# Optimization experiments

Measured on AMD Instinct MI355X. Metric: run time of the kernel, lower is better.

Reference implementation:

```python
import jax, jax.numpy as jnp
import numpy as np

DIM = 1024
HEADS = 8
DIM_HEAD = 64
INNER = HEADS * DIM_HEAD  # 512


def setup_inputs() -> dict:
    key = jax.random.key(0)
    k1, k2, k3, k4 = jax.random.split(key, 4)
    x = jax.random.normal(k1, (4, 4096, DIM), dtype=jnp.float32)
    W_qkv = jax.random.normal(k2, (DIM, 3 * INNER), dtype=jnp.float32) * (DIM ** -0.5)
    W_out = jax.random.normal(k3, (INNER, DIM), dtype=jnp.float32) * (INNER ** -0.5)
    b_out = jax.random.normal(k4, (DIM,), dtype=jnp.float32) * 0.01
    return {"x": x, "W_qkv": W_qkv, "W_out": W_out, "b_out": b_out}


def reference(x, W_qkv, W_out, b_out):
    b, n, _ = x.shape
    qkv = x @ W_qkv                                   # [b, n, 3*inner]
    q, k, v = jnp.split(qkv, 3, axis=-1)              # each [b, n, inner]

    def to_heads(t):
        return t.reshape(b, n, HEADS, DIM_HEAD).transpose(0, 2, 1, 3)  # [b, h, n, d]

    q = jax.nn.elu(to_heads(q)) + 1.0
    k = jax.nn.elu(to_heads(k)) + 1.0
    v = to_heads(v)
    # kv summary matrix: [b, h, d, e]
    context = jnp.einsum('bhnd,bhne->bhde', k, v)
    out = jnp.einsum('bhde,bhnd->bhne', context, q)   # [b, h, n, e]
    out = out.transpose(0, 2, 1, 3).reshape(b, n, INNER)
    return out @ W_out + b_out
```

## Files before the change

kernel.cpp:

```cpp
#include <hip/hip_runtime.h>
#include <hip/hip_bf16.h>
#include <cstdint>

typedef __attribute__((ext_vector_type(4))) float f32x4;
typedef __attribute__((ext_vector_type(8))) short bf16x8;

__device__ __forceinline__ ushort f2bf(float f) {
  unsigned u = __builtin_bit_cast(unsigned, f);
  u += 0x7fffu + ((u >> 16) & 1u);
  return (ushort)(u >> 16);
}

__device__ __forceinline__ void gload_lds16(const ushort* g, ushort* l) {
  __builtin_amdgcn_global_load_lds(
      (const __attribute__((address_space(1))) unsigned int*)g,
      (__attribute__((address_space(3))) unsigned int*)l, 16, 0, 0);
}

__device__ __forceinline__ void hard_barrier() {
  __builtin_amdgcn_sched_barrier(0);
  __builtin_amdgcn_s_barrier();
  __builtin_amdgcn_sched_barrier(0);
}

template <int N>
__device__ __forceinline__ void wait_vm() {
  if constexpr (N == 0) asm volatile("s_waitcnt vmcnt(0)" ::: "memory");
  else if constexpr (N == 2) asm volatile("s_waitcnt vmcnt(2)" ::: "memory");
  else if constexpr (N == 4) asm volatile("s_waitcnt vmcnt(4)" ::: "memory");
  else if constexpr (N == 6) asm volatile("s_waitcnt vmcnt(6)" ::: "memory");
  else static_assert(N < 0, "unsupported vmcnt");
}

__device__ __forceinline__ float elu1(float v) {
  return (v > 0.f) ? (v + 1.f) : __expf(v);
}

__global__ __launch_bounds__(256) void prep_kernel(const float4* __restrict__ x,
                                                   ushort4* __restrict__ xb,
                                                   const float* __restrict__ W,
                                                   ushort* __restrict__ Wt) {
  if (blockIdx.x < 2048) {
    const int n4 = 16384 * 1024 / 4;
    const int stride = 2048 * 256;
    for (int i = blockIdx.x * 256 + threadIdx.x; i < n4; i += stride) {
      float4 f = x[i];
      ushort4 o;
      o.x = f2bf(f.x); o.y = f2bf(f.y); o.z = f2bf(f.z); o.w = f2bf(f.w);
      xb[i] = o;
    }
  } else {
    __shared__ float tile[32][33];
    const int tb = blockIdx.x - 2048;
    const int n0 = (tb % 48) * 32;
    const int k0 = (tb / 48) * 32;
    const int tx = threadIdx.x & 31;
    const int ty = threadIdx.x >> 5;
    #pragma unroll
    for (int p = 0; p < 4; ++p) {
      int k = k0 + ty + p * 8;
      tile[ty + p * 8][tx] = W[(size_t)k * 1536 + n0 + tx];
    }
    __syncthreads();
    #pragma unroll
    for (int p = 0; p < 4; ++p) {
      int n = n0 + ty + p * 8;
      Wt[(size_t)n * 1024 + k0 + tx] = f2bf(tile[tx][ty + p * 8]);
    }
  }
}

template <int LDA, int LDB, int NT>
__device__ __forceinline__ void gemm_core(const ushort* __restrict__ A,
                                          const ushort* __restrict__ Bt,
                                          int row0, int col0, f32x4 acc[4][4],
                                          ushort* lds) {
  const int tid = threadIdx.x;
  const int l = tid & 63;
  const int wid = tid >> 6;
  const int fr = l & 15;
  const int fq = l >> 4;
  const int wr = wid >> 2;
  const int wc = wid & 3;

  const int scol = ((l & 7) * 8) ^ (((l >> 3) & 7) * 8);
  const ushort* aS = A + (size_t)(row0 + (tid >> 3)) * LDA + scol;
  const ushort* bS = Bt + (size_t)(col0 + (tid >> 3)) * LDB + scol;

  int aRow[4], bRow[4], kx[2];
  #pragma unroll
  for (int m = 0; m < 4; ++m) aRow[m] = (wr * 64 + m * 16 + fr) * 64;
  #pragma unroll
  for (int n = 0; n < 4; ++n) bRow[n] = (wc * 64 + n * 16 + fr) * 64;
  #pragma unroll
  for (int ks = 0; ks < 2; ++ks) kx[ks] = (ks * 32 + fq * 8) ^ ((fr & 7) * 8);

  auto stage = [&](int t) {
    ushort* dst = lds + (t % 3) * 24576 + tid * 8;
    const int ko = t * 64;
    #pragma unroll
    for (int p = 0; p < 2; ++p)
      gload_lds16(aS + (size_t)(p * 64) * LDA + ko, dst + p * 4096);
    #pragma unroll
    for (int p = 0; p < 4; ++p)
      gload_lds16(bS + (size_t)(p * 64) * LDB + ko, dst + 8192 + p * 4096);
  };

  stage(0);
  stage(1);
  wait_vm<6>();
  hard_barrier();

  #pragma unroll
  for (int t = 0; t < NT; ++t) {
    if (t + 2 < NT) stage(t + 2);
    const ushort* aB = lds + (t % 3) * 24576;
    const ushort* bB = aB + 8192;
    #pragma unroll
    for (int ks = 0; ks < 2; ++ks) {
      bf16x8 av[4], bv[4];
      #pragma unroll
      for (int m = 0; m < 4; ++m) av[m] = *(const bf16x8*)&aB[aRow[m] + kx[ks]];
      #pragma unroll
      for (int n = 0; n < 4; ++n) bv[n] = *(const bf16x8*)&bB[bRow[n] + kx[ks]];
      __builtin_amdgcn_s_setprio(1);
      #pragma unroll
      for (int m = 0; m < 4; ++m)
        #pragma unroll
        for (int n = 0; n < 4; ++n)
          acc[m][n] = __builtin_amdgcn_mfma_f32_16x16x32_bf16(av[m], bv[n], acc[m][n], 0, 0, 0);
      __builtin_amdgcn_s_setprio(0);
    }
    if (t + 2 < NT) {
      wait_vm<6>();
      hard_barrier();
    } else if (t + 1 < NT) {
      wait_vm<0>();
      hard_barrier();
    }
  }
}

__global__ __launch_bounds__(512, 2) void gemm_qkv_kernel(const ushort* __restrict__ xb,
                                                          const ushort* __restrict__ wt,
                                                          ushort* __restrict__ q,
                                                          ushort* __restrict__ kT,
                                                          ushort* __restrict__ vT) {
  __shared__ ushort lds[73728];
  f32x4 acc[4][4] = {};
  const int row0 = blockIdx.x * 128;
  const int col0 = blockIdx.y * 256;
  gemm_core<1024, 1024, 16>(xb, wt, row0, col0, acc, lds);
  const int l = threadIdx.x & 63;
  const int wid = threadIdx.x >> 6;
  const int wr = wid >> 2, wc = wid & 3;
  const int fr = l & 15, fq = l >> 4;
  #pragma unroll
  for (int m = 0; m < 4; ++m) {
    #pragma unroll
    for (int n = 0; n < 4; ++n) {
      const int c = col0 + wc * 64 + n * 16 + fr;
      const int r0 = row0 + wr * 64 + m * 16 + fq * 4;
      if (c < 512) {
        #pragma unroll
        for (int j = 0; j < 4; ++j)
          q[(size_t)(r0 + j) * 512 + c] = f2bf(elu1(acc[m][n][j]));
      } else if (c < 1024) {
        const int d = c - 512;
        const int bh = (r0 >> 12) * 8 + (d >> 6);
        const int nn = r0 & 4095;
        ushort4 o;
        o.x = f2bf(elu1(acc[m][n][0]));
        o.y = f2bf(elu1(acc[m][n][1]));
        o.z = f2bf(elu1(acc[m][n][2]));
        o.w = f2bf(elu1(acc[m][n][3]));
        *(ushort4*)&kT[((size_t)bh * 64 + (d & 63)) * 4096 + nn] = o;
      } else {
        const int d = c - 1024;
        const int bh = (r0 >> 12) * 8 + (d >> 6);
        const int nn = r0 & 4095;
        ushort4 o;
        o.x = f2bf(acc[m][n][0]);
        o.y = f2bf(acc[m][n][1]);
        o.z = f2bf(acc[m][n][2]);
        o.w = f2bf(acc[m][n][3]);
        *(ushort4*)&vT[((size_t)bh * 64 + (d & 63)) * 4096 + nn] = o;
      }
    }
  }
}

__global__ __launch_bounds__(256) void ctx_mfma_kernel(const ushort* __restrict__ kT,
                                                       const ushort* __restrict__ vT,
                                                       float* __restrict__ part) {
  __shared__ ushort lds[16384];
  const int bh = blockIdx.x;
  const int sp = blockIdx.y;
  const int tid = threadIdx.x;
  const int l = tid & 63, wid = tid >> 6;
  const int fr = l & 15, fq = l >> 4;
  const int wr = wid >> 1, wc = wid & 1;

  const size_t base = (size_t)bh * 64 * 4096 + sp * 512;
  const int srow = tid >> 2;
  const int lam = (tid & 3) ^ ((tid >> 3) & 3);
  const ushort* aG = kT + base + (size_t)srow * 4096 + lam * 8;
  const ushort* bG = vT + base + (size_t)srow * 4096 + lam * 8;

  auto stage = [&](int t) {
    ushort* d = lds + (t & 3) * 4096 + tid * 8;
    gload_lds16(aG + t * 32, d);
    gload_lds16(bG + t * 32, d + 2048);
  };

  const int sig = fq ^ ((fr >> 1) & 3);
  f32x4 acc[2][2] = {};

  auto compute = [&](int t) {
    const ushort* sb = lds + (t & 3) * 4096;
    bf16x8 av[2], bv[2];
    #pragma unroll
    for (int mm = 0; mm < 2; ++mm)
      av[mm] = *(const bf16x8*)&sb[(wr * 32 + mm * 16 + fr) * 32 + sig * 8];
    #pragma unroll
    for (int nn = 0; nn < 2; ++nn)
      bv[nn] = *(const bf16x8*)&sb[2048 + (wc * 32 + nn * 16 + fr) * 32 + sig * 8];
    #pragma unroll
    for (int mm = 0; mm < 2; ++mm)
      #pragma unroll
      for (int nn = 0; nn < 2; ++nn)
        acc[mm][nn] = __builtin_amdgcn_mfma_f32_16x16x32_bf16(av[mm], bv[nn], acc[mm][nn], 0, 0, 0);
  };

  constexpr int NT = 16;
  stage(0); stage(1); stage(2);
  for (int t = 0; t < NT; ++t) {
    if (t <= NT - 3) wait_vm<4>();
    else if (t == NT - 2) wait_vm<2>();
    else wait_vm<0>();
    hard_barrier();
    compute(t);
    hard_barrier();
    if (t + 3 < NT) stage(t + 3);
  }

  float* dst = part + ((size_t)sp * 32 + bh) * 4096;
  #pragma unroll
  for (int mm = 0; mm < 2; ++mm)
    #pragma unroll
    for (int nn = 0; nn < 2; ++nn)
      #pragma unroll
      for (int j = 0; j < 4; ++j)
        dst[(wr * 32 + mm * 16 + fq * 4 + j) * 64 + wc * 32 + nn * 16 + fr] = acc[mm][nn][j];
}

__global__ __launch_bounds__(256) void weff_kernel(const float* __restrict__ part,
                                                   const float* __restrict__ Wout,
                                                   ushort* __restrict__ weff) {
  const int bh = blockIdx.x;
  const int h = bh & 7;
  const int m0 = blockIdx.y * 128;
  const int t = threadIdx.x;
  __shared__ float cs[64 * 64];
  __shared__ float ws[64][128];
  #pragma unroll
  for (int p = 0; p < 4; ++p) {
    const int idx = p * 1024 + t * 4;
    f32x4 s = {};
    #pragma unroll
    for (int sp = 0; sp < 8; ++sp)
      s += *(const f32x4*)&part[(size_t)sp * 131072 + (size_t)bh * 4096 + idx];
    *(f32x4*)&cs[idx] = s;
  }
  #pragma unroll
  for (int p = 0; p < 8; ++p) {
    const int e = (t >> 5) + p * 8;
    const int c = (t & 31) * 4;
    *(float4*)&ws[e][c] = *(const float4*)&Wout[(size_t)(h * 64 + e) * 1024 + m0 + c];
  }
  __syncthreads();
  const int m = t & 127;
  const int dh = (t >> 7) * 32;
  float acc[32] = {};
  for (int e = 0; e < 64; ++e) {
    const float w = ws[e][m];
    #pragma unroll
    for (int i = 0; i < 32; ++i)
      acc[i] += cs[(dh + i) * 64 + e] * w;
  }
  ushort* dst = weff + ((size_t)(bh >> 3) * 1024 + m0 + m) * 512 + h * 64 + dh;
  #pragma unroll
  for (int i = 0; i < 32; ++i) dst[i] = f2bf(acc[i]);
}

__global__ __launch_bounds__(512, 2) void gemm_out_kernel(const ushort* __restrict__ q,
                                                          const ushort* __restrict__ weff,
                                                          const float* __restrict__ bout,
                                                          float* __restrict__ out) {
  __shared__ ushort lds[73728];
  f32x4 acc[4][4] = {};
  const int row0 = blockIdx.x * 128;
  const int col0 = blockIdx.y * 256;
  const int b = row0 >> 12;
  gemm_core<512, 512, 8>(q, weff + (size_t)b * 1024 * 512, row0, col0, acc, lds);
  const int l = threadIdx.x & 63;
  const int wid = threadIdx.x >> 6;
  const int wr = wid >> 2, wc = wid & 3;
  const int fr = l & 15, fq = l >> 4;
  #pragma unroll
  for (int m = 0; m < 4; ++m) {
    #pragma unroll
    for (int n = 0; n < 4; ++n) {
      const int c = col0 + wc * 64 + n * 16 + fr;
      const float bb = bout[c];
      #pragma unroll
      for (int j = 0; j < 4; ++j) {
        const int r = row0 + wr * 64 + m * 16 + fq * 4 + j;
        out[(size_t)r * 1024 + c] = acc[m][n][j] + bb;
      }
    }
  }
}

extern "C" void kernel_launch(void* const* d_in, const int* in_sizes, int n_in,
                              void* d_out, int out_size, void* d_ws, size_t ws_size,
                              hipStream_t stream) {
  const float* x    = (const float*)d_in[0];
  const float* Wqkv = (const float*)d_in[1];
  const float* Wout = (const float*)d_in[2];
  const float* bout = (const float*)d_in[3];
  float* out = (float*)d_out;
  char* ws = (char*)d_ws;

  ushort* xb   = (ushort*)(ws);
  float*  part = (float* )(ws);
  ushort* wt   = (ushort*)(ws + 33554432);
  ushort* q    = (ushort*)(ws + 36700160);
  ushort* kT   = (ushort*)(ws + 53477376);
  ushort* vT   = (ushort*)(ws + 70254592);
  ushort* weff = (ushort*)(ws + 87556096);

  prep_kernel<<<3584, 256, 0, stream>>>((const float4*)x, (ushort4*)xb, Wqkv, wt);
  gemm_qkv_kernel<<<dim3(128, 6), 512, 0, stream>>>(xb, wt, q, kT, vT);
  ctx_mfma_kernel<<<dim3(32, 8), 256, 0, stream>>>(kT, vT, part);
  weff_kernel<<<dim3(32, 8), 256, 0, stream>>>(part, Wout, weff);
  gemm_out_kernel<<<dim3(128, 4), 512, 0, stream>>>(q, weff, bout, out);
}
```

Measured before the change: 128.7 us.

## Fuse fp32-to-bf16 conversion of x into QKV GEMM A-tile loading

Removes the separate pass that converts x to bf16 in the workspace. The QKV GEMM now loads fp32 x through registers, converts to bf16 and writes into swizzled LDS, while B still streams directly to LDS via global_load_lds, using a triple-buffered pipeline. This avoids writing and re-reading a 32MB bf16 copy of x. In exchange, each GEMM block reads twice as many bytes for A (6 column blocks each reread fp32 x), and register-staged A loads add VGPR pressure and wait points.

```diff
diff --git a/kernel.cpp b/kernel.cpp
--- a/kernel.cpp
+++ b/kernel.cpp
@@ -11,6 +11,10 @@
   return (ushort)(u >> 16);
 }
 
+__device__ __forceinline__ unsigned cvt2(float a, float b) {
+  return (unsigned)f2bf(a) | ((unsigned)f2bf(b) << 16);
+}
+
 __device__ __forceinline__ void gload_lds16(const ushort* g, ushort* l) {
   __builtin_amdgcn_global_load_lds(
       (const __attribute__((address_space(1))) unsigned int*)g,
@@ -21,6 +25,10 @@
   __builtin_amdgcn_sched_barrier(0);
   __builtin_amdgcn_s_barrier();
   __builtin_amdgcn_sched_barrier(0);
+}
+
+__device__ __forceinline__ void wait_lgkm0() {
+  asm volatile("s_waitcnt lgkmcnt(0)" ::: "memory");
 }
 
 template <int N>
@@ -29,6 +37,7 @@
   else if constexpr (N == 2) asm volatile("s_waitcnt vmcnt(2)" ::: "memory");
   else if constexpr (N == 4) asm volatile("s_waitcnt vmcnt(4)" ::: "memory");
   else if constexpr (N == 6) asm volatile("s_waitcnt vmcnt(6)" ::: "memory");
+  else if constexpr (N == 8) asm volatile("s_waitcnt vmcnt(8)" ::: "memory");
   else static_assert(N < 0, "unsupported vmcnt");
 }
 
@@ -36,37 +45,23 @@
   return (v > 0.f) ? (v + 1.f) : __expf(v);
 }
 
-__global__ __launch_bounds__(256) void prep_kernel(const float4* __restrict__ x,
-                                                   ushort4* __restrict__ xb,
-                                                   const float* __restrict__ W,
-                                                   ushort* __restrict__ Wt) {
-  if (blockIdx.x < 2048) {
-    const int n4 = 16384 * 1024 / 4;
-    const int stride = 2048 * 256;
-    for (int i = blockIdx.x * 256 + threadIdx.x; i < n4; i += stride) {
-      float4 f = x[i];
-      ushort4 o;
-      o.x = f2bf(f.x); o.y = f2bf(f.y); o.z = f2bf(f.z); o.w = f2bf(f.w);
-      xb[i] = o;
-    }
-  } else {
-    __shared__ float tile[32][33];
-    const int tb = blockIdx.x - 2048;
-    const int n0 = (tb % 48) * 32;
-    const int k0 = (tb / 48) * 32;
-    const int tx = threadIdx.x & 31;
-    const int ty = threadIdx.x >> 5;
-    #pragma unroll
-    for (int p = 0; p < 4; ++p) {
-      int k = k0 + ty + p * 8;
-      tile[ty + p * 8][tx] = W[(size_t)k * 1536 + n0 + tx];
-    }
-    __syncthreads();
-    #pragma unroll
-    for (int p = 0; p < 4; ++p) {
-      int n = n0 + ty + p * 8;
-      Wt[(size_t)n * 1024 + k0 + tx] = f2bf(tile[tx][ty + p * 8]);
-    }
+__global__ __launch_bounds__(256) void transpose_w_kernel(const float* __restrict__ W,
+                                                          ushort* __restrict__ Wt) {
+  __shared__ float tile[32][33];
+  int n0 = blockIdx.x * 32;
+  int k0 = blockIdx.y * 32;
+  int tx = threadIdx.x;
+  int ty = threadIdx.y;
+  #pragma unroll
+  for (int p = 0; p < 4; ++p) {
+    int k = k0 + ty + p * 8;
+    tile[ty + p * 8][tx] = W[(size_t)k * 1536 + n0 + tx];
+  }
+  __syncthreads();
+  #pragma unroll
+  for (int p = 0; p < 4; ++p) {
+    int n = n0 + ty + p * 8;
+    Wt[(size_t)n * 1024 + k0 + tx] = f2bf(tile[tx][ty + p * 8]);
   }
 }
 
@@ -141,20 +136,108 @@
   }
 }
 
-__global__ __launch_bounds__(512, 2) void gemm_qkv_kernel(const ushort* __restrict__ xb,
+__global__ __launch_bounds__(512, 2) void gemm_qkv_kernel(const float* __restrict__ x,
                                                           const ushort* __restrict__ wt,
                                                           ushort* __restrict__ q,
                                                           ushort* __restrict__ kT,
                                                           ushort* __restrict__ vT) {
   __shared__ ushort lds[73728];
+  constexpr int LDA = 1024, LDB = 1024, NT = 16;
   f32x4 acc[4][4] = {};
   const int row0 = blockIdx.x * 128;
   const int col0 = blockIdx.y * 256;
-  gemm_core<1024, 1024, 16>(xb, wt, row0, col0, acc, lds);
-  const int l = threadIdx.x & 63;
-  const int wid = threadIdx.x >> 6;
-  const int wr = wid >> 2, wc = wid & 3;
-  const int fr = l & 15, fq = l >> 4;
+
+  const int tid = threadIdx.x;
+  const int l = tid & 63;
+  const int wid = tid >> 6;
+  const int fr = l & 15;
+  const int fq = l >> 4;
+  const int wr = wid >> 2;
+  const int wc = wid & 3;
+
+  const int scol = ((l & 7) * 8) ^ (((l >> 3) & 7) * 8);
+  const float* aS = x + (size_t)(row0 + (tid >> 3)) * LDA + scol;
+  const ushort* bS = wt + (size_t)(col0 + (tid >> 3)) * LDB + scol;
+
+  int aRow[4], bRow[4], kx[2];
+  #pragma unroll
+  for (int m = 0; m < 4; ++m) aRow[m] = (wr * 64 + m * 16 + fr) * 64;
+  #pragma unroll
+  for (int n = 0; n < 4; ++n) bRow[n] = (wc * 64 + n * 16 + fr) * 64;
+  #pragma unroll
+  for (int ks = 0; ks < 2; ++ks) kx[ks] = (ks * 32 + fq * 8) ^ ((fr & 7) * 8);
+
+  float4 va[2][4];
+
+  auto issueT = [&](int t) {
+    const float* s = aS + t * 64;
+    #pragma unroll
+    for (int p = 0; p < 2; ++p) {
+      va[t & 1][p * 2]     = *(const float4*)(s + (size_t)(p * 64) * LDA);
+      va[t & 1][p * 2 + 1] = *(const float4*)(s + (size_t)(p * 64) * LDA + 4);
+    }
+    ushort* dst = lds + (t % 3) * 24576 + 8192 + tid * 8;
+    const int ko = t * 64;
+    #pragma unroll
+    for (int p = 0; p < 4; ++p)
+      gload_lds16(bS + (size_t)(p * 64) * LDB + ko, dst + p * 4096);
+  };
+
+  auto writeA = [&](int t) {
+    ushort* dst = lds + (t % 3) * 24576 + tid * 8;
+    #pragma unroll
+    for (int p = 0; p < 2; ++p) {
+      const float4 lo = va[t & 1][p * 2];
+      const float4 hi = va[t & 1][p * 2 + 1];
+      uint4 w;
+      w.x = cvt2(lo.x, lo.y);
+      w.y = cvt2(lo.z, lo.w);
+      w.z = cvt2(hi.x, hi.y);
+      w.w = cvt2(hi.z, hi.w);
+      *(uint4*)(dst + p * 4096) = w;
+    }
+  };
+
+  auto compute = [&](int t) {
+    const ushort* aB = lds + (t % 3) * 24576;
+    const ushort* bB = aB + 8192;
+    #pragma unroll
+    for (int ks = 0; ks < 2; ++ks) {
+      bf16x8 av[4], bv[4];
+      #pragma unroll
+      for (int m = 0; m < 4; ++m) av[m] = *(const bf16x8*)&aB[aRow[m] + kx[ks]];
+      #pragma unroll
+      for (int n = 0; n < 4; ++n) bv[n] = *(const bf16x8*)&bB[bRow[n] + kx[ks]];
+      __builtin_amdgcn_s_setprio(1);
+      #pragma unroll
+      for (int m = 0; m < 4; ++m)
+        #pragma unroll
+        for (int n = 0; n < 4; ++n)
+          acc[m][n] = __builtin_amdgcn_mfma_f32_16x16x32_bf16(av[m], bv[n], acc[m][n], 0, 0, 0);
+      __builtin_amdgcn_s_setprio(0);
+    }
+  };
+
+  issueT(0);
+  issueT(1);
+  wait_vm<8>();
+  writeA(0);
+  wait_lgkm0();
+  hard_barrier();
+
+  #pragma unroll
+  for (int t = 0; t < NT; ++t) {
+    if (t + 2 < NT) issueT(t + 2);
+    compute(t);
+    if (t + 1 < NT) {
+      if (t + 2 < NT) wait_vm<8>();
+      else wait_vm<0>();
+      writeA(t + 1);
+      wait_lgkm0();
+      hard_barrier();
+    }
+  }
+
   #pragma unroll
   for (int m = 0; m < 4; ++m) {
     #pragma unroll
@@ -332,7 +415,6 @@
   float* out = (float*)d_out;
   char* ws = (char*)d_ws;
 
-  ushort* xb   = (ushort*)(ws);
   float*  part = (float* )(ws);
   ushort* wt   = (ushort*)(ws + 33554432);
   ushort* q    = (ushort*)(ws + 36700160);
@@ -340,8 +422,8 @@
   ushort* vT   = (ushort*)(ws + 70254592);
   ushort* weff = (ushort*)(ws + 87556096);
 
-  prep_kernel<<<3584, 256, 0, stream>>>((const float4*)x, (ushort4*)xb, Wqkv, wt);
-  gemm_qkv_kernel<<<dim3(128, 6), 512, 0, stream>>>(xb, wt, q, kT, vT);
+  transpose_w_kernel<<<dim3(48, 32), dim3(32, 8), 0, stream>>>(Wqkv, wt);
+  gemm_qkv_kernel<<<dim3(128, 6), 512, 0, stream>>>(x, wt, q, kT, vT);
   ctx_mfma_kernel<<<dim3(32, 8), 256, 0, stream>>>(kT, vT, part);
   weff_kernel<<<dim3(32, 8), 256, 0, stream>>>(part, Wout, weff);
   gemm_out_kernel<<<dim3(128, 4), 512, 0, stream>>>(q, weff, bout, out);
```

Result: slower. 148.7 us (+15.5%).

## Halve GEMM K-tile to 32 with new LDS swizzle to raise occupancy

Applied to the files above, without the earlier changes.

Rewrites the shared GEMM core to stage K-tiles of 32 instead of 64, which halves the LDS footprint per block (about 72KB instead of 144KB) and uses a new XOR swizzle for the smaller tile. Launch bounds go from 2 to 4 blocks per CU so more waves can hide latency, and both GEMM kernels now run twice as many K iterations. The trade-off is more barriers and waits per unit of MFMA work, plus added register pressure from the higher occupancy target, which may force spills with a 64-float accumulator.

```diff
diff --git a/kernel.cpp b/kernel.cpp
--- a/kernel.cpp
+++ b/kernel.cpp
@@ -27,8 +27,8 @@
 __device__ __forceinline__ void wait_vm() {
   if constexpr (N == 0) asm volatile("s_waitcnt vmcnt(0)" ::: "memory");
   else if constexpr (N == 2) asm volatile("s_waitcnt vmcnt(2)" ::: "memory");
+  else if constexpr (N == 3) asm volatile("s_waitcnt vmcnt(3)" ::: "memory");
   else if constexpr (N == 4) asm volatile("s_waitcnt vmcnt(4)" ::: "memory");
-  else if constexpr (N == 6) asm volatile("s_waitcnt vmcnt(6)" ::: "memory");
   else static_assert(N < 0, "unsupported vmcnt");
 }
 
@@ -71,10 +71,10 @@
 }
 
 template <int LDA, int LDB, int NT>
-__device__ __forceinline__ void gemm_core(const ushort* __restrict__ A,
-                                          const ushort* __restrict__ Bt,
-                                          int row0, int col0, f32x4 acc[4][4],
-                                          ushort* lds) {
+__device__ __forceinline__ void gemm_core32(const ushort* __restrict__ A,
+                                            const ushort* __restrict__ Bt,
+                                            int row0, int col0, f32x4 acc[4][4],
+                                            ushort* lds) {
   const int tid = threadIdx.x;
   const int l = tid & 63;
   const int wid = tid >> 6;
@@ -83,56 +83,48 @@
   const int wr = wid >> 2;
   const int wc = wid & 3;
 
-  const int scol = ((l & 7) * 8) ^ (((l >> 3) & 7) * 8);
-  const ushort* aS = A + (size_t)(row0 + (tid >> 3)) * LDA + scol;
-  const ushort* bS = Bt + (size_t)(col0 + (tid >> 3)) * LDB + scol;
-
-  int aRow[4], bRow[4], kx[2];
-  #pragma unroll
-  for (int m = 0; m < 4; ++m) aRow[m] = (wr * 64 + m * 16 + fr) * 64;
-  #pragma unroll
-  for (int n = 0; n < 4; ++n) bRow[n] = (wc * 64 + n * 16 + fr) * 64;
-  #pragma unroll
-  for (int ks = 0; ks < 2; ++ks) kx[ks] = (ks * 32 + fq * 8) ^ ((fr & 7) * 8);
+  const int sc = ((tid & 3) ^ ((tid >> 2) & 3)) * 8;
+  const ushort* aS = A + (size_t)(row0 + (tid >> 2)) * LDA + sc;
+  const ushort* bS = Bt + (size_t)(col0 + (tid >> 2)) * LDB + sc;
 
   auto stage = [&](int t) {
-    ushort* dst = lds + (t % 3) * 24576 + tid * 8;
-    const int ko = t * 64;
-    #pragma unroll
-    for (int p = 0; p < 2; ++p)
-      gload_lds16(aS + (size_t)(p * 64) * LDA + ko, dst + p * 4096);
-    #pragma unroll
-    for (int p = 0; p < 4; ++p)
-      gload_lds16(bS + (size_t)(p * 64) * LDB + ko, dst + 8192 + p * 4096);
+    ushort* base = lds + (t % 3) * 12288 + tid * 8;
+    gload_lds16(aS + t * 32, base);
+    gload_lds16(bS + t * 32, base + 4096);
+    gload_lds16(bS + (size_t)128 * LDB + t * 32, base + 8192);
+  };
+
+  const int sig = fq ^ (fr & 3);
+  const int aOff = wr * 2048 + fr * 32 + sig * 8;
+  const int bOff = 4096 + wc * 2048 + fr * 32 + sig * 8;
+
+  auto compute = [&](int t) {
+    const ushort* sb = lds + (t % 3) * 12288;
+    bf16x8 av[4], bv[4];
+    #pragma unroll
+    for (int m = 0; m < 4; ++m) av[m] = *(const bf16x8*)(sb + aOff + m * 512);
+    #pragma unroll
+    for (int n = 0; n < 4; ++n) bv[n] = *(const bf16x8*)(sb + bOff + n * 512);
+    __builtin_amdgcn_s_setprio(1);
+    #pragma unroll
+    for (int m = 0; m < 4; ++m)
+      #pragma unroll
+      for (int n = 0; n < 4; ++n)
+        acc[m][n] = __builtin_amdgcn_mfma_f32_16x16x32_bf16(av[m], bv[n], acc[m][n], 0, 0, 0);
+    __builtin_amdgcn_s_setprio(0);
   };
 
   stage(0);
   stage(1);
-  wait_vm<6>();
+  wait_vm<3>();
   hard_barrier();
 
-  #pragma unroll
+  #pragma unroll 3
   for (int t = 0; t < NT; ++t) {
     if (t + 2 < NT) stage(t + 2);
-    const ushort* aB = lds + (t % 3) * 24576;
-    const ushort* bB = aB + 8192;
-    #pragma unroll
-    for (int ks = 0; ks < 2; ++ks) {
-      bf16x8 av[4], bv[4];
-      #pragma unroll
-      for (int m = 0; m < 4; ++m) av[m] = *(const bf16x8*)&aB[aRow[m] + kx[ks]];
-      #pragma unroll
-      for (int n = 0; n < 4; ++n) bv[n] = *(const bf16x8*)&bB[bRow[n] + kx[ks]];
-      __builtin_amdgcn_s_setprio(1);
-      #pragma unroll
-      for (int m = 0; m < 4; ++m)
-        #pragma unroll
-        for (int n = 0; n < 4; ++n)
-          acc[m][n] = __builtin_amdgcn_mfma_f32_16x16x32_bf16(av[m], bv[n], acc[m][n], 0, 0, 0);
-      __builtin_amdgcn_s_setprio(0);
-    }
+    compute(t);
     if (t + 2 < NT) {
-      wait_vm<6>();
+      wait_vm<3>();
       hard_barrier();
     } else if (t + 1 < NT) {
       wait_vm<0>();
@@ -141,16 +133,16 @@
   }
 }
 
-__global__ __launch_bounds__(512, 2) void gemm_qkv_kernel(const ushort* __restrict__ xb,
+__global__ __launch_bounds__(512, 4) void gemm_qkv_kernel(const ushort* __restrict__ xb,
                                                           const ushort* __restrict__ wt,
                                                           ushort* __restrict__ q,
                                                           ushort* __restrict__ kT,
                                                           ushort* __restrict__ vT) {
-  __shared__ ushort lds[73728];
+  __shared__ ushort lds[36864];
   f32x4 acc[4][4] = {};
   const int row0 = blockIdx.x * 128;
   const int col0 = blockIdx.y * 256;
-  gemm_core<1024, 1024, 16>(xb, wt, row0, col0, acc, lds);
+  gemm_core32<1024, 1024, 32>(xb, wt, row0, col0, acc, lds);
   const int l = threadIdx.x & 63;
   const int wid = threadIdx.x >> 6;
   const int wr = wid >> 2, wc = wid & 3;
@@ -293,16 +285,16 @@
   for (int i = 0; i < 32; ++i) dst[i] = f2bf(acc[i]);
 }
 
-__global__ __launch_bounds__(512, 2) void gemm_out_kernel(const ushort* __restrict__ q,
+__global__ __launch_bounds__(512, 4) void gemm_out_kernel(const ushort* __restrict__ q,
                                                           const ushort* __restrict__ weff,
                                                           const float* __restrict__ bout,
                                                           float* __restrict__ out) {
-  __shared__ ushort lds[73728];
+  __shared__ ushort lds[36864];
   f32x4 acc[4][4] = {};
   const int row0 = blockIdx.x * 128;
   const int col0 = blockIdx.y * 256;
   const int b = row0 >> 12;
-  gemm_core<512, 512, 8>(q, weff + (size_t)b * 1024 * 512, row0, col0, acc, lds);
+  gemm_core32<512, 512, 16>(q, weff + (size_t)b * 1024 * 512, row0, col0, acc, lds);
   const int l = threadIdx.x & 63;
   const int wid = threadIdx.x >> 6;
   const int wr = wid >> 2, wc = wid & 3;
```

Measured after the change: 127.8 us. Within noise of the previous version (-0.7%).
